# Performance work log

Measured on AMD Instinct MI355X. Metric: run time of the kernel, lower is better.

## Reference

```python
import jax, jax.numpy as jnp
import numpy as np
import math

B, S, D, H = 2, 2048, 1024, 16
DK = D // H


def setup_inputs() -> dict:
    key = jax.random.key(0)
    ks = jax.random.split(key, 12)
    s = 1.0 / math.sqrt(D)
    inp = {
        "q": jax.random.normal(ks[0], (B, S, D), jnp.float32),
        "k": jax.random.normal(ks[1], (B, S, D), jnp.float32),
        "v": jax.random.normal(ks[2], (B, S, D), jnp.float32),
        "mask": jnp.broadcast_to(jnp.tril(jnp.ones((S, S), jnp.int32))[None, None], (B, 1, S, S)),
        "Wq": jax.random.normal(ks[3], (D, D), jnp.float32) * s,
        "bq": jnp.zeros((D,), jnp.float32),
        "Wk": jax.random.normal(ks[4], (D, D), jnp.float32) * s,
        "bk": jnp.zeros((D,), jnp.float32),
        "Wv": jax.random.normal(ks[5], (D, D), jnp.float32) * s,
        "bv": jnp.zeros((D,), jnp.float32),
        "Wo": jax.random.normal(ks[6], (D, D), jnp.float32) * s,
        "bo": jnp.zeros((D,), jnp.float32),
    }
    return inp


def reference(q, k, v, mask, Wq, bq, Wk, bk, Wv, bv, Wo, bo):
    b = q.shape[0]
    # project and split heads -> [b, h, s, d_k]
    def heads(x, W, bias):
        y = x @ W.T + bias
        return y.reshape(b, -1, H, DK).transpose(0, 2, 1, 3)
    qh = heads(q, Wq, bq)
    kh = heads(k, Wk, bk)
    vh = heads(v, Wv, bv)
    scores = jnp.einsum("bhqd,bhkd->bhqk", qh, kh) / math.sqrt(DK)
    scores = jnp.where(mask == 0, jnp.float32(-1e9), scores)
    weights = jax.nn.softmax(scores, axis=-1)  # dropout p=0 -> identity
    out = jnp.einsum("bhqk,bhkd->bhqd", weights, vh)
    out = out.transpose(0, 2, 1, 3).reshape(b, -1, H * DK)
    return out @ Wo.T + bo
```

## Files before the change

### kernel.cpp

```cpp
#include <hip/hip_runtime.h>

#define B_ 2
#define S_ 2048
#define D_ 1024
#define H_ 16
#define DK_ 64
#define M_ 4096

typedef unsigned short u16;
typedef __bf16 bf16x8 __attribute__((ext_vector_type(8)));
typedef float floatx4 __attribute__((ext_vector_type(4)));

#if __has_builtin(__builtin_amdgcn_exp2f)
#define EXP2F(x) __builtin_amdgcn_exp2f(x)
#else
#define EXP2F(x) exp2f(x)
#endif

__device__ __forceinline__ u16 f2bf(float f) {
  unsigned u = __float_as_uint(f);
  u += 0x7fffu + ((u >> 16) & 1u);
  return (u16)(u >> 16);
}

__device__ __forceinline__ void stage16(const void* g, void* l) {
  __builtin_amdgcn_global_load_lds(
      (const __attribute__((address_space(1))) unsigned int*)g,
      (__attribute__((address_space(3))) unsigned int*)l, 16, 0, 0);
}

__global__ __launch_bounds__(256) void cvt_all_kernel(
    const float* __restrict__ q, const float* __restrict__ k, const float* __restrict__ v,
    const float* __restrict__ wq, const float* __restrict__ wk,
    const float* __restrict__ wv, const float* __restrict__ wo,
    u16* dq, u16* dk, u16* dv, u16* dwq, u16* dwk, u16* dwv, u16* dwo) {
  const float* s; u16* d; size_t base;
  const int bx = blockIdx.x;
  if (bx < 6144) {
    const int t0 = bx >> 11;
    base = (size_t)(bx & 2047) * 2048;
    s = t0 == 0 ? q : t0 == 1 ? k : v;
    d = t0 == 0 ? dq : t0 == 1 ? dk : dv;
  } else {
    const int t0 = (bx - 6144) >> 9;
    base = (size_t)((bx - 6144) & 511) * 2048;
    s = t0 == 0 ? wq : t0 == 1 ? wk : t0 == 2 ? wv : wo;
    d = t0 == 0 ? dwq : t0 == 1 ? dwk : t0 == 2 ? dwv : dwo;
  }
  const size_t i = base + (size_t)threadIdx.x * 8;
  const float4 f0 = *reinterpret_cast<const float4*>(s + i);
  const float4 f1 = *reinterpret_cast<const float4*>(s + i + 4);
  union { u16 h[8]; uint4 u; } cv;
  cv.h[0] = f2bf(f0.x); cv.h[1] = f2bf(f0.y); cv.h[2] = f2bf(f0.z); cv.h[3] = f2bf(f0.w);
  cv.h[4] = f2bf(f1.x); cv.h[5] = f2bf(f1.y); cv.h[6] = f2bf(f1.z); cv.h[7] = f2bf(f1.w);
  *reinterpret_cast<uint4*>(d + i) = cv.u;
}

template <int BN>
__device__ __forceinline__ void gemm_body(
    const u16* __restrict__ A, const u16* __restrict__ W,
    const float* __restrict__ bias, void* __restrict__ outp,
    int mode, float scale, int kbeg, int kend) {
  constexpr int NT = BN / 32;
  constexpr int NB = BN / 32;
  __shared__ __align__(16) u16 As[128 * 64];
  __shared__ __align__(16) u16 Bs[BN * 64];

  const int t = threadIdx.x;
  const int lane = t & 63, w = t >> 6;
  const int quad = lane >> 4, l16 = lane & 15;
  const int wm = w >> 1, wn = w & 1;
  const int m0 = blockIdx.y * 128, n0 = blockIdx.x * BN;

  const u16 *gA[4], *gB[NB]; u16 *lA[4], *lB[NB];
#pragma unroll
  for (int i = 0; i < 4; i++) {
    const int ch = (i * 4 + w) * 64 + lane;
    const int row = ch >> 3, c = ch & 7, cs = c ^ (row & 7);
    gA[i] = A + (size_t)(m0 + row) * 1024 + cs * 8;
    lA[i] = As + ((i * 4 + w) * 64) * 8;
  }
#pragma unroll
  for (int i = 0; i < NB; i++) {
    const int ch = (i * 4 + w) * 64 + lane;
    const int row = ch >> 3, c = ch & 7, cs = c ^ (row & 7);
    gB[i] = W + (size_t)(n0 + row) * 1024 + cs * 8;
    lB[i] = Bs + ((i * 4 + w) * 64) * 8;
  }

  floatx4 acc[4][NT] = {};

  for (int k0 = kbeg; k0 < kend; k0 += 64) {
    __syncthreads();
#pragma unroll
    for (int i = 0; i < 4; i++) stage16(gA[i] + k0, lA[i]);
#pragma unroll
    for (int i = 0; i < NB; i++) stage16(gB[i] + k0, lB[i]);
    __syncthreads();
#pragma unroll
    for (int kk = 0; kk < 2; kk++) {
      bf16x8 af[4], bf[NT];
      const int sw = (kk * 4 + quad) ^ (l16 & 7);
#pragma unroll
      for (int mt = 0; mt < 4; mt++) {
        const int row = wm * 64 + mt * 16 + l16;
        af[mt] = *reinterpret_cast<const bf16x8*>(&As[(row * 8 + sw) * 8]);
      }
#pragma unroll
      for (int nt = 0; nt < NT; nt++) {
        const int row = wn * (NT * 16) + nt * 16 + l16;
        bf[nt] = *reinterpret_cast<const bf16x8*>(&Bs[(row * 8 + sw) * 8]);
      }
#pragma unroll
      for (int mt = 0; mt < 4; mt++)
#pragma unroll
        for (int nt = 0; nt < NT; nt++)
          acc[mt][nt] = __builtin_amdgcn_mfma_f32_16x16x32_bf16(af[mt], bf[nt], acc[mt][nt], 0, 0, 0);
    }
  }

#pragma unroll
  for (int mt = 0; mt < 4; mt++) {
    const int mbase = m0 + wm * 64 + mt * 16 + quad * 4;
    const int bb = mbase >> 11, s0v = mbase & 2047;
#pragma unroll
    for (int nt = 0; nt < NT; nt++) {
      const int n = n0 + wn * (NT * 16) + nt * 16 + l16;
      const float bvv = (mode == 4 && kbeg != 0) ? 0.f : bias[n];
      if (mode == 0) {
        u16* Y = (u16*)outp;
        const int h = n >> 6, dk = n & 63;
#pragma unroll
        for (int r = 0; r < 4; r++)
          Y[(((size_t)(bb * H_ + h)) * S_ + (s0v + r)) * DK_ + dk] =
              f2bf((acc[mt][nt][r] + bvv) * scale);
      } else if (mode == 2) {
        u16* Y = (u16*)outp;
        const int h = n >> 6, dk = n & 63;
        union { u16 h4[4]; uint2 u; } pk2;
#pragma unroll
        for (int r = 0; r < 4; r++) pk2.h4[r] = f2bf(acc[mt][nt][r] + bvv);
        *reinterpret_cast<uint2*>(
            &Y[(((size_t)(bb * H_ + h)) * DK_ + dk) * S_ + s0v]) = pk2.u;
      } else {
        float* Y = (float*)outp;
#pragma unroll
        for (int r = 0; r < 4; r++)
          unsafeAtomicAdd(&Y[(size_t)(mbase + r) * 1024 + n], acc[mt][nt][r] + bvv);
      }
    }
  }
}

__global__ __launch_bounds__(256) void qkv_gemm_kernel(
    const u16* qa, const u16* ka, const u16* va,
    const u16* wq, const u16* wk, const u16* wv,
    const float* bq, const float* bk, const float* bv,
    u16* Qh, u16* Kh, u16* VhT) {
  const int g = blockIdx.z;
  const u16* A = g == 0 ? qa : g == 1 ? ka : va;
  const u16* W = g == 0 ? wq : g == 1 ? wk : wv;
  const float* bias = g == 0 ? bq : g == 1 ? bk : bv;
  void* out = g == 0 ? (void*)Qh : g == 1 ? (void*)Kh : (void*)VhT;
  gemm_body<128>(A, W, bias, out, g == 2 ? 2 : 0,
                 g == 0 ? 0.18033688011112f : 1.0f, 0, 1024);
}

__global__ __launch_bounds__(256) void o_gemm_kernel(
    const u16* ctx, const u16* wo, const float* bo, float* out) {
  gemm_body<64>(ctx, wo, bo, out, 4, 1.0f, blockIdx.z * 512, blockIdx.z * 512 + 512);
}

__global__ __launch_bounds__(256) void attn_kernel(
    const u16* __restrict__ Qh, const u16* __restrict__ Kh,
    const u16* __restrict__ VhT, u16* __restrict__ Ctx) {
  __shared__ __align__(16) u16 Kt[64 * 64];
  __shared__ __align__(16) u16 Vt[64 * 64];
  __shared__ __align__(16) u16 Ps[64 * 72];

  const int t = threadIdx.x;
  const int lane = t & 63, w = t >> 6;
  const int quad = lane >> 4, l16 = lane & 15;

  const int bh = blockIdx.x & 31;
  const int i = blockIdx.x >> 5;
  const int j = i >> 3, r0 = i & 7;
  const int u = (j == 0) ? 31 - r0 : (j == 1) ? r0 : (j == 2) ? 23 - r0 : 8 + r0;
  const int qb = u * 64;
  const int ntile = u + 1;

  const u16* Qp = Qh + (size_t)bh * S_ * DK_;
  const u16* Kp = Kh + (size_t)bh * S_ * DK_;
  const u16* Vp = VhT + (size_t)bh * DK_ * S_;

  bf16x8 bq[2];
#pragma unroll
  for (int kk = 0; kk < 2; kk++)
    bq[kk] = *reinterpret_cast<const bf16x8*>(
        &Qp[(size_t)(qb + w * 16 + l16) * DK_ + kk * 32 + quad * 8]);

  const u16 *gK[2], *gV[2]; u16 *lK[2], *lV[2];
#pragma unroll
  for (int i2 = 0; i2 < 2; i2++) {
    const int ch = (i2 * 4 + w) * 64 + lane;
    const int row = ch >> 3, c = ch & 7, cs = c ^ (row & 7);
    gK[i2] = Kp + (size_t)row * DK_ + cs * 8;
    gV[i2] = Vp + (size_t)row * S_ + cs * 8;
    lK[i2] = Kt + ((i2 * 4 + w) * 64) * 8;
    lV[i2] = Vt + ((i2 * 4 + w) * 64) * 8;
  }

  float l_run = 0.f;
  floatx4 o[4] = {};
  const int qg = qb + w * 16 + l16;

  for (int it = 0; it < ntile; it++) {
    const int j0 = it * 64;
    __syncthreads();
#pragma unroll
    for (int i2 = 0; i2 < 2; i2++) {
      stage16(gK[i2] + (size_t)j0 * DK_, lK[i2]);
      stage16(gV[i2] + j0, lV[i2]);
    }
    __syncthreads();

    floatx4 sc[4] = {};
#pragma unroll
    for (int mt = 0; mt < 4; mt++) {
      const int row = mt * 16 + l16;
#pragma unroll
      for (int kk = 0; kk < 2; kk++) {
        const bf16x8 ak = *reinterpret_cast<const bf16x8*>(
            &Kt[(row * 8 + ((kk * 4 + quad) ^ (l16 & 7))) * 8]);
        sc[mt] = __builtin_amdgcn_mfma_f32_16x16x32_bf16(ak, bq[kk], sc[mt], 0, 0, 0);
      }
    }

    const bool maskT = (it == ntile - 1);
    float psum = 0.f;
#pragma unroll
    for (int mt = 0; mt < 4; mt++) {
      float p[4];
#pragma unroll
      for (int r = 0; r < 4; r++) {
        float vsc = sc[mt][r];
        if (maskT && (j0 + mt * 16 + quad * 4 + r > qg)) vsc = -1e30f;
        p[r] = EXP2F(vsc);
        psum += p[r];
      }
      uint2 pu;
      pu.x = (__float_as_uint(p[1]) & 0xffff0000u) | (__float_as_uint(p[0]) >> 16);
      pu.y = (__float_as_uint(p[3]) & 0xffff0000u) | (__float_as_uint(p[2]) >> 16);
      *reinterpret_cast<uint2*>(&Ps[(w * 16 + l16) * 72 + mt * 16 + quad * 4]) = pu;
    }
    psum += __shfl_xor(psum, 16);
    psum += __shfl_xor(psum, 32);
    l_run += psum;

#pragma unroll
    for (int kk = 0; kk < 2; kk++) {
      const bf16x8 ap = *reinterpret_cast<const bf16x8*>(
          &Ps[(w * 16 + l16) * 72 + kk * 32 + quad * 8]);
#pragma unroll
      for (int nt = 0; nt < 4; nt++) {
        const bf16x8 bv = *reinterpret_cast<const bf16x8*>(
            &Vt[((nt * 16 + l16) * 8 + ((kk * 4 + quad) ^ (l16 & 7))) * 8]);
        o[nt] = __builtin_amdgcn_mfma_f32_16x16x32_bf16(ap, bv, o[nt], 0, 0, 0);
      }
    }
  }

  const int bb = bh >> 4, hh = bh & 15;
#pragma unroll
  for (int r = 0; r < 4; r++) {
    const float lr = __shfl(l_run, quad * 4 + r);
    const float inv = 1.0f / lr;
    const int srow = qb + w * 16 + quad * 4 + r;
    u16* cp = Ctx + ((size_t)bb * S_ + srow) * D_ + hh * DK_;
#pragma unroll
    for (int nt = 0; nt < 4; nt++)
      cp[nt * 16 + l16] = f2bf(o[nt][r] * inv);
  }
}

extern "C" void kernel_launch(void* const* d_in, const int* in_sizes, int n_in,
                              void* d_out, int out_size, void* d_ws, size_t ws_size,
                              hipStream_t stream) {
  const float* q  = (const float*)d_in[0];
  const float* k  = (const float*)d_in[1];
  const float* v  = (const float*)d_in[2];
  const float* Wq = (const float*)d_in[4];
  const float* bq = (const float*)d_in[5];
  const float* Wk = (const float*)d_in[6];
  const float* bk = (const float*)d_in[7];
  const float* Wv = (const float*)d_in[8];
  const float* bv = (const float*)d_in[9];
  const float* Wo = (const float*)d_in[10];
  const float* bo = (const float*)d_in[11];

  const size_t nW = (size_t)D_ * D_;
  const size_t nA = (size_t)M_ * D_;
  u16* wqb = (u16*)d_ws;
  u16* wkb = wqb + nW;
  u16* wvb = wkb + nW;
  u16* wob = wvb + nW;
  u16* qb_ = wob + nW;
  u16* kb_ = qb_ + nA;
  u16* vb_ = kb_ + nA;
  u16* Qh  = vb_ + nA;
  u16* Kh  = Qh + nA;
  u16* VhT = Kh + nA;
  u16* Ctx = qb_;

  hipMemsetAsync(d_out, 0, (size_t)out_size * sizeof(float), stream);

  cvt_all_kernel<<<dim3(8192), 256, 0, stream>>>(q, k, v, Wq, Wk, Wv, Wo,
                                                 qb_, kb_, vb_, wqb, wkb, wvb, wob);

  qkv_gemm_kernel<<<dim3(D_ / 128, M_ / 128, 3), 256, 0, stream>>>(
      qb_, kb_, vb_, wqb, wkb, wvb, bq, bk, bv, Qh, Kh, VhT);

  attn_kernel<<<dim3(B_ * H_ * (S_ / 64)), 256, 0, stream>>>(Qh, Kh, VhT, Ctx);

  o_gemm_kernel<<<dim3(D_ / 64, M_ / 128, 2), 256, 0, stream>>>(Ctx, wob, bo, (float*)d_out);
}
```

Measured before the change: 269.0 us.

## Double-buffer LDS tiles in GEMM and attention; fold output memset into convert kernel

The QKV/O GEMM and the attention kernel now keep two LDS buffers. Each iteration issues the async global-to-LDS load for the next K/V or A/B tile while computing on the current one, and one barrier per iteration is gone. The separate hipMemsetAsync of the output is replaced by extra blocks in the conversion kernel that write zeros. This aims to hide global load latency and save a launch, at the cost of doubling LDS usage, which may lower occupancy. It also depends on the barrier waiting for the outstanding LDS-DMA loads before the current tile is read.

```diff
diff --git a/kernel.cpp b/kernel.cpp
--- a/kernel.cpp
+++ b/kernel.cpp
@@ -33,9 +33,17 @@
     const float* __restrict__ q, const float* __restrict__ k, const float* __restrict__ v,
     const float* __restrict__ wq, const float* __restrict__ wk,
     const float* __restrict__ wv, const float* __restrict__ wo,
-    u16* dq, u16* dk, u16* dv, u16* dwq, u16* dwk, u16* dwv, u16* dwo) {
+    u16* dq, u16* dk, u16* dv, u16* dwq, u16* dwk, u16* dwv, u16* dwo,
+    float* dout) {
+  const int bx = blockIdx.x;
+  if (bx >= 8192) {
+    const size_t i = ((size_t)(bx - 8192) * 256 + threadIdx.x) * 8;
+    const uint4 z = {0, 0, 0, 0};
+    *reinterpret_cast<uint4*>(dout + i) = z;
+    *reinterpret_cast<uint4*>(dout + i + 4) = z;
+    return;
+  }
   const float* s; u16* d; size_t base;
-  const int bx = blockIdx.x;
   if (bx < 6144) {
     const int t0 = bx >> 11;
     base = (size_t)(bx & 2047) * 2048;
@@ -63,8 +71,8 @@
     int mode, float scale, int kbeg, int kend) {
   constexpr int NT = BN / 32;
   constexpr int NB = BN / 32;
-  __shared__ __align__(16) u16 As[128 * 64];
-  __shared__ __align__(16) u16 Bs[BN * 64];
+  __shared__ __align__(16) u16 As[2][128 * 64];
+  __shared__ __align__(16) u16 Bs[2][BN * 64];
 
   const int t = threadIdx.x;
   const int lane = t & 63, w = t >> 6;
@@ -78,25 +86,33 @@
     const int ch = (i * 4 + w) * 64 + lane;
     const int row = ch >> 3, c = ch & 7, cs = c ^ (row & 7);
     gA[i] = A + (size_t)(m0 + row) * 1024 + cs * 8;
-    lA[i] = As + ((i * 4 + w) * 64) * 8;
+    lA[i] = As[0] + ((i * 4 + w) * 64) * 8;
   }
 #pragma unroll
   for (int i = 0; i < NB; i++) {
     const int ch = (i * 4 + w) * 64 + lane;
     const int row = ch >> 3, c = ch & 7, cs = c ^ (row & 7);
     gB[i] = W + (size_t)(n0 + row) * 1024 + cs * 8;
-    lB[i] = Bs + ((i * 4 + w) * 64) * 8;
+    lB[i] = Bs[0] + ((i * 4 + w) * 64) * 8;
   }
 
   floatx4 acc[4][NT] = {};
 
+#pragma unroll
+  for (int i = 0; i < 4; i++) stage16(gA[i] + kbeg, lA[i]);
+#pragma unroll
+  for (int i = 0; i < NB; i++) stage16(gB[i] + kbeg, lB[i]);
+
   for (int k0 = kbeg; k0 < kend; k0 += 64) {
+    const int cur = ((k0 - kbeg) >> 6) & 1;
+    const int nxt = cur ^ 1;
     __syncthreads();
-#pragma unroll
-    for (int i = 0; i < 4; i++) stage16(gA[i] + k0, lA[i]);
-#pragma unroll
-    for (int i = 0; i < NB; i++) stage16(gB[i] + k0, lB[i]);
-    __syncthreads();
+    if (k0 + 64 < kend) {
+#pragma unroll
+      for (int i = 0; i < 4; i++) stage16(gA[i] + k0 + 64, lA[i] + nxt * 128 * 64);
+#pragma unroll
+      for (int i = 0; i < NB; i++) stage16(gB[i] + k0 + 64, lB[i] + nxt * BN * 64);
+    }
 #pragma unroll
     for (int kk = 0; kk < 2; kk++) {
       bf16x8 af[4], bf[NT];
@@ -104,12 +120,12 @@
 #pragma unroll
       for (int mt = 0; mt < 4; mt++) {
         const int row = wm * 64 + mt * 16 + l16;
-        af[mt] = *reinterpret_cast<const bf16x8*>(&As[(row * 8 + sw) * 8]);
+        af[mt] = *reinterpret_cast<const bf16x8*>(&As[cur][(row * 8 + sw) * 8]);
       }
 #pragma unroll
       for (int nt = 0; nt < NT; nt++) {
         const int row = wn * (NT * 16) + nt * 16 + l16;
-        bf[nt] = *reinterpret_cast<const bf16x8*>(&Bs[(row * 8 + sw) * 8]);
+        bf[nt] = *reinterpret_cast<const bf16x8*>(&Bs[cur][(row * 8 + sw) * 8]);
       }
 #pragma unroll
       for (int mt = 0; mt < 4; mt++)
@@ -174,8 +190,8 @@
 __global__ __launch_bounds__(256) void attn_kernel(
     const u16* __restrict__ Qh, const u16* __restrict__ Kh,
     const u16* __restrict__ VhT, u16* __restrict__ Ctx) {
-  __shared__ __align__(16) u16 Kt[64 * 64];
-  __shared__ __align__(16) u16 Vt[64 * 64];
+  __shared__ __align__(16) u16 Kt[2][64 * 64];
+  __shared__ __align__(16) u16 Vt[2][64 * 64];
   __shared__ __align__(16) u16 Ps[64 * 72];
 
   const int t = threadIdx.x;
@@ -206,23 +222,32 @@
     const int row = ch >> 3, c = ch & 7, cs = c ^ (row & 7);
     gK[i2] = Kp + (size_t)row * DK_ + cs * 8;
     gV[i2] = Vp + (size_t)row * S_ + cs * 8;
-    lK[i2] = Kt + ((i2 * 4 + w) * 64) * 8;
-    lV[i2] = Vt + ((i2 * 4 + w) * 64) * 8;
+    lK[i2] = Kt[0] + ((i2 * 4 + w) * 64) * 8;
+    lV[i2] = Vt[0] + ((i2 * 4 + w) * 64) * 8;
   }
 
   float l_run = 0.f;
   floatx4 o[4] = {};
   const int qg = qb + w * 16 + l16;
 
+#pragma unroll
+  for (int i2 = 0; i2 < 2; i2++) {
+    stage16(gK[i2], lK[i2]);
+    stage16(gV[i2], lV[i2]);
+  }
+
   for (int it = 0; it < ntile; it++) {
+    const int cur = it & 1, nxt = cur ^ 1;
+    __syncthreads();
+    if (it + 1 < ntile) {
+      const int j1 = (it + 1) * 64;
+#pragma unroll
+      for (int i2 = 0; i2 < 2; i2++) {
+        stage16(gK[i2] + (size_t)j1 * DK_, lK[i2] + nxt * 64 * 64);
+        stage16(gV[i2] + j1, lV[i2] + nxt * 64 * 64);
+      }
+    }
     const int j0 = it * 64;
-    __syncthreads();
-#pragma unroll
-    for (int i2 = 0; i2 < 2; i2++) {
-      stage16(gK[i2] + (size_t)j0 * DK_, lK[i2]);
-      stage16(gV[i2] + j0, lV[i2]);
-    }
-    __syncthreads();
 
     floatx4 sc[4] = {};
 #pragma unroll
@@ -231,7 +256,7 @@
 #pragma unroll
       for (int kk = 0; kk < 2; kk++) {
         const bf16x8 ak = *reinterpret_cast<const bf16x8*>(
-            &Kt[(row * 8 + ((kk * 4 + quad) ^ (l16 & 7))) * 8]);
+            &Kt[cur][(row * 8 + ((kk * 4 + quad) ^ (l16 & 7))) * 8]);
         sc[mt] = __builtin_amdgcn_mfma_f32_16x16x32_bf16(ak, bq[kk], sc[mt], 0, 0, 0);
       }
     }
@@ -264,7 +289,7 @@
 #pragma unroll
       for (int nt = 0; nt < 4; nt++) {
         const bf16x8 bv = *reinterpret_cast<const bf16x8*>(
-            &Vt[((nt * 16 + l16) * 8 + ((kk * 4 + quad) ^ (l16 & 7))) * 8]);
+            &Vt[cur][((nt * 16 + l16) * 8 + ((kk * 4 + quad) ^ (l16 & 7))) * 8]);
         o[nt] = __builtin_amdgcn_mfma_f32_16x16x32_bf16(ap, bv, o[nt], 0, 0, 0);
       }
     }
@@ -312,10 +337,9 @@
   u16* VhT = Kh + nA;
   u16* Ctx = qb_;
 
-  hipMemsetAsync(d_out, 0, (size_t)out_size * sizeof(float), stream);
-
-  cvt_all_kernel<<<dim3(8192), 256, 0, stream>>>(q, k, v, Wq, Wk, Wv, Wo,
-                                                 qb_, kb_, vb_, wqb, wkb, wvb, wob);
+  cvt_all_kernel<<<dim3(10240), 256, 0, stream>>>(q, k, v, Wq, Wk, Wv, Wo,
+                                                  qb_, kb_, vb_, wqb, wkb, wvb, wob,
+                                                  (float*)d_out);
 
   qkv_gemm_kernel<<<dim3(D_ / 128, M_ / 128, 3), 256, 0, stream>>>(
       qb_, kb_, vb_, wqb, wkb, wvb, bq, bk, bv, Qh, Kh, VhT);
```

After: 266.0 us. No clear change (-1.1%).
